# Performance work log

Measured on AMD Instinct MI355X. Metric: run time of the kernel, lower is better.

## Reference

```python
import jax, jax.numpy as jnp
import numpy as np

N_NODES = 100000
N_EDGES = 600000
NODE_DIM = 128
EDGE_DIM = 16
OUT_DIM = 128


def setup_inputs() -> dict:
    key = jax.random.key(0)
    k1, k2, k3, k4 = jax.random.split(key, 4)
    x = jax.random.normal(k1, (N_NODES, NODE_DIM), dtype=jnp.float32)
    edge_index = jax.random.randint(k2, (2, N_EDGES), 0, N_NODES, dtype=jnp.int64)
    edge_attr = jax.random.normal(k3, (N_EDGES, EDGE_DIM), dtype=jnp.float32)
    in_dim = 2 * NODE_DIM + EDGE_DIM
    # Linear layer params (Kaiming-uniform-like scale)
    lim = 1.0 / np.sqrt(in_dim)
    W = jax.random.uniform(k4, (in_dim, OUT_DIM), minval=-lim, maxval=lim, dtype=jnp.float32)
    b = jnp.zeros((OUT_DIM,), dtype=jnp.float32)
    return {"x": x, "edge_index": edge_index, "edge_attr": edge_attr, "W": W, "b": b}


def reference(x, edge_index, edge_attr, W, b):
    # h_ij = Linear([h_i, h_j, x_ij])
    h_i = x[edge_index[0]]            # [E, node_dim]
    h_j = x[edge_index[1]]            # [E, node_dim]
    # Split the GEMM over the concat blocks to avoid materializing [E, 2D+F]
    W_i, W_j, W_e = W[:NODE_DIM], W[NODE_DIM:2 * NODE_DIM], W[2 * NODE_DIM:]
    out = h_i @ W_i + h_j @ W_j + edge_attr @ W_e + b
    return out  # [E, out_dim]
```

## Files before the change

kernel.cpp:

```cpp
#include <hip/hip_runtime.h>
#include <cstdint>
#include <cstddef>

#define NE 600000
#define NN 100000

typedef __attribute__((ext_vector_type(8)))  __bf16         bf16x8;
typedef __attribute__((ext_vector_type(16))) float          f32x16;
typedef __attribute__((ext_vector_type(8)))  unsigned short u16x8;
typedef __attribute__((ext_vector_type(2)))  float          f32x2;

__device__ inline unsigned short f2bf(float f) {
    unsigned int u = __builtin_bit_cast(unsigned int, f);
    u += 0x7fffu + ((u >> 16) & 1u);
    return (unsigned short)(u >> 16);
}

__global__ void pack_w(const float* __restrict__ W, unsigned short* __restrict__ Wp) {
    int t = blockIdx.x * 256 + threadIdx.x;
    if (t >= 272 * 128) return;
    int k = t >> 7, col = t & 127;
    Wp[((k >> 3) * 128 + col) * 8 + (k & 7)] = f2bf(W[t]);
}

__global__ void cvt_x(const float* __restrict__ x, unsigned short* __restrict__ xb) {
    size_t t = (size_t)(blockIdx.x * 256 + threadIdx.x) * 8;
    float4 a = *(const float4*)(x + t);
    float4 b = *(const float4*)(x + t + 4);
    u16x8 o;
    o[0] = f2bf(a.x); o[1] = f2bf(a.y); o[2] = f2bf(a.z); o[3] = f2bf(a.w);
    o[4] = f2bf(b.x); o[5] = f2bf(b.y); o[6] = f2bf(b.z); o[7] = f2bf(b.w);
    *(u16x8*)(xb + t) = o;
}


__global__ __launch_bounds__(256, 2) void node_mm(
    const float* __restrict__ x,
    const unsigned short* __restrict__ Wp,
    float* __restrict__ Y,
    float* __restrict__ Z)
{
    const int lane = threadIdx.x & 63;
    const int wave = threadIdx.x >> 6;
    const int r = lane & 31;
    const int h = lane >> 5;
    const int nb = (blockIdx.x * 4 + wave) * 32;
    if (nb >= NN) return;

    const bf16x8* Wg = (const bf16x8*)Wp;
    f32x16 accY[4], accZ[4];
#pragma unroll
    for (int t = 0; t < 4; ++t)
#pragma unroll
        for (int i = 0; i < 16; ++i) { accY[t][i] = 0.f; accZ[t][i] = 0.f; }

    const float4* ax4 = (const float4*)(x + (size_t)(nb + r) * 128);
#pragma unroll
    for (int S = 0; S < 8; ++S) {
        const int kb = 2 * S + h;
        float4 pp = ax4[kb * 2], qq = ax4[kb * 2 + 1];
        u16x8 o;
        o[0] = f2bf(pp.x); o[1] = f2bf(pp.y); o[2] = f2bf(pp.z); o[3] = f2bf(pp.w);
        o[4] = f2bf(qq.x); o[5] = f2bf(qq.y); o[6] = f2bf(qq.z); o[7] = f2bf(qq.w);
        bf16x8 a = __builtin_bit_cast(bf16x8, o);
#pragma unroll
        for (int t = 0; t < 4; ++t) {
            accY[t] = __builtin_amdgcn_mfma_f32_32x32x16_bf16(
                          a, Wg[kb * 128 + t * 32 + r],        accY[t], 0, 0, 0);
            accZ[t] = __builtin_amdgcn_mfma_f32_32x32x16_bf16(
                          a, Wg[(16 + kb) * 128 + t * 32 + r], accZ[t], 0, 0, 0);
        }
    }

#pragma unroll
    for (int t = 0; t < 4; ++t)
#pragma unroll
        for (int i = 0; i < 16; ++i) {
            int row = (i & 3) + 8 * (i >> 2) + 4 * h;
            Y[(size_t)(nb + row) * 128 + t * 32 + r] = accY[t][i];
            Z[(size_t)(nb + row) * 128 + t * 32 + r] = accZ[t][i];
        }
}

__global__ __launch_bounds__(256, 4) void edge_combine(
    const float* __restrict__ Y,
    const float* __restrict__ Z,
    const int*   __restrict__ ei,
    const float* __restrict__ ea,
    const float* __restrict__ W,
    const float* __restrict__ bias,
    float* __restrict__ out)
{
    const int lane = threadIdx.x & 63;
    const int w = (blockIdx.x * 256 + threadIdx.x) >> 6;
    if (w >= NE / 64) return;
    const int ebase = w * 64;

    f32x2 we[16];
#pragma unroll
    for (int k = 0; k < 16; ++k)
        we[k] = *(const f32x2*)(W + (size_t)(256 + k) * 128 + 2 * lane);
    const f32x2 bv = *(const f32x2*)(bias + 2 * lane);

    const int srcv = ei[ebase + lane];
    const int dstv = ei[NE + ebase + lane];

    int raw[16];
#pragma unroll
    for (int m = 0; m < 16; ++m)
        raw[m] = __builtin_bit_cast(int,
                     ea[(size_t)ebase * 16 + m * 64 + lane]);

    f32x2 yv[8], zv[8];
#pragma unroll
    for (int i = 0; i < 8; ++i) {
        int s = __builtin_amdgcn_readlane(srcv, i);
        int d = __builtin_amdgcn_readlane(dstv, i);
        yv[i] = *(const f32x2*)(Y + ((size_t)s << 7) + 2 * lane);
        zv[i] = *(const f32x2*)(Z + ((size_t)d << 7) + 2 * lane);
    }

#pragma unroll
    for (int j = 0; j < 64; ++j) {
        const int slot = j & 7;
        f32x2 y = yv[slot], z = zv[slot];
        if (j + 8 < 64) {
            int s = __builtin_amdgcn_readlane(srcv, j + 8);
            int d = __builtin_amdgcn_readlane(dstv, j + 8);
            yv[slot] = *(const f32x2*)(Y + ((size_t)s << 7) + 2 * lane);
            zv[slot] = *(const f32x2*)(Z + ((size_t)d << 7) + 2 * lane);
        }
        f32x2 acc = bv;
#pragma unroll
        for (int k = 0; k < 16; ++k) {
            float e = __builtin_bit_cast(float,
                          __builtin_amdgcn_readlane(raw[j >> 2], (j & 3) * 16 + k));
            acc = acc + we[k] * e;
        }
        f32x2 o = acc + y + z;
        __builtin_nontemporal_store(
            o, (f32x2*)(out + ((size_t)(ebase + j) << 7) + 2 * lane));
    }
}


#define WAIT_VM(n) do { asm volatile("" ::: "memory");                      \
                        __builtin_amdgcn_s_waitcnt(0x0F70 | (n));           \
                        asm volatile("" ::: "memory"); } while (0)

__global__ __launch_bounds__(256, 2) void edge_mm2(
    const unsigned short* __restrict__ xb,
    const unsigned short* __restrict__ Wp,
    const int* __restrict__ ei,
    const float* __restrict__ ea,
    const float* __restrict__ bias,
    float* __restrict__ out)
{
    __shared__ __attribute__((aligned(16))) unsigned short Abuf[4][2][32][128];

    const int lane = threadIdx.x & 63;
    const int wave = threadIdx.x >> 6;
    const int r  = lane & 31;
    const int h  = lane >> 5;
    const int g4 = lane >> 4;
    const int sl = lane & 15;
    const int ebase = blockIdx.x * 128 + wave * 32;
    if (ebase >= NE) return;
    const int e = ebase + r;

#pragma unroll
    for (int i = 0; i < 8; ++i) {
        int row = 4 * i + g4;
        int nidx = ei[ebase + row];
        const unsigned short* gs = xb + (size_t)nidx * 128 + ((sl ^ (row & 15)) << 3);
        __builtin_amdgcn_global_load_lds(
            (const __attribute__((address_space(1))) void*)gs,
            (__attribute__((address_space(3))) void*)&Abuf[wave][0][4 * i][0],
            16, 0, 0);
    }
#pragma unroll
    for (int i = 0; i < 8; ++i) {
        int row = 4 * i + g4;
        int nidx = ei[NE + ebase + row];
        const unsigned short* gs = xb + (size_t)nidx * 128 + ((sl ^ (row & 15)) << 3);
        __builtin_amdgcn_global_load_lds(
            (const __attribute__((address_space(1))) void*)gs,
            (__attribute__((address_space(3))) void*)&Abuf[wave][1][4 * i][0],
            16, 0, 0);
    }

    const float4* ae = (const float4*)(ea + (size_t)e * 16);
    float4 p = ae[2 * h], q = ae[2 * h + 1];

    f32x16 acc[4];
#pragma unroll
    for (int t = 0; t < 4; ++t)
#pragma unroll
        for (int i = 0; i < 16; ++i) acc[t][i] = 0.f;

    const bf16x8* Wg = (const bf16x8*)Wp;
    const int rm = r & 15;

    WAIT_VM(8);
#pragma unroll
    for (int S = 0; S < 8; ++S) {
        int kb = 2 * S + h;
        bf16x8 a = *(const bf16x8*)&Abuf[wave][0][r][(kb ^ rm) << 3];
#pragma unroll
        for (int t = 0; t < 4; ++t) {
            bf16x8 b = Wg[kb * 128 + t * 32 + r];
            acc[t] = __builtin_amdgcn_mfma_f32_32x32x16_bf16(a, b, acc[t], 0, 0, 0);
        }
    }

    WAIT_VM(0);
#pragma unroll
    for (int S = 0; S < 8; ++S) {
        int kb = 2 * S + h;
        bf16x8 a = *(const bf16x8*)&Abuf[wave][1][r][(kb ^ rm) << 3];
#pragma unroll
        for (int t = 0; t < 4; ++t) {
            bf16x8 b = Wg[(16 + kb) * 128 + t * 32 + r];
            acc[t] = __builtin_amdgcn_mfma_f32_32x32x16_bf16(a, b, acc[t], 0, 0, 0);
        }
    }

    {
        u16x8 o;
        o[0] = f2bf(p.x); o[1] = f2bf(p.y); o[2] = f2bf(p.z); o[3] = f2bf(p.w);
        o[4] = f2bf(q.x); o[5] = f2bf(q.y); o[6] = f2bf(q.z); o[7] = f2bf(q.w);
        bf16x8 a = __builtin_bit_cast(bf16x8, o);
#pragma unroll
        for (int t = 0; t < 4; ++t) {
            bf16x8 b = Wg[(32 + h) * 128 + t * 32 + r];
            acc[t] = __builtin_amdgcn_mfma_f32_32x32x16_bf16(a, b, acc[t], 0, 0, 0);
        }
    }

    float* orow = out + (size_t)ebase * 128;
#pragma unroll
    for (int t = 0; t < 4; ++t) {
        float bv = bias[t * 32 + r];
#pragma unroll
        for (int i = 0; i < 16; ++i) {
            int row = (i & 3) + 8 * (i >> 2) + 4 * h;
            orow[(size_t)row * 128 + t * 32 + r] = acc[t][i] + bv;
        }
    }
}

__global__ __launch_bounds__(256, 2) void edge_mm_fb(
    const float* __restrict__ x,
    const unsigned short* __restrict__ Wp,
    const int* __restrict__ ei,
    const float* __restrict__ ea,
    const float* __restrict__ bias,
    float* __restrict__ out)
{
    __shared__ unsigned short Wl[32 * 128 * 8];
    {
        const uint4* Wg = (const uint4*)Wp;
        uint4* Ws = (uint4*)Wl;
#pragma unroll
        for (int i = 0; i < 16; ++i)
            Ws[threadIdx.x + 256 * i] = Wg[threadIdx.x + 256 * i];
    }
    const int lane = threadIdx.x & 63;
    const int wave = threadIdx.x >> 6;
    const int r = lane & 31;
    const int h = lane >> 5;
    const long ebase = (long)blockIdx.x * 128 + wave * 32;
    __syncthreads();
    if (ebase >= NE) return;
    const int e = (int)ebase + r;
    const int src = ei[e];
    const int dst = ei[NE + e];
    f32x16 acc[4];
#pragma unroll
    for (int t = 0; t < 4; ++t)
#pragma unroll
        for (int i = 0; i < 16; ++i) acc[t][i] = 0.f;
    const bf16x8* Wv = (const bf16x8*)Wl;
#pragma unroll
    for (int ph = 0; ph < 2; ++ph) {
        int node = ph ? dst : src;
#pragma unroll
        for (int s = 0; s < 8; ++s) {
            const float4* ax = (const float4*)(x + (size_t)node * 128);
            float4 pp = ax[(2 * s + h) * 2], qq = ax[(2 * s + h) * 2 + 1];
            u16x8 o;
            o[0] = f2bf(pp.x); o[1] = f2bf(pp.y); o[2] = f2bf(pp.z); o[3] = f2bf(pp.w);
            o[4] = f2bf(qq.x); o[5] = f2bf(qq.y); o[6] = f2bf(qq.z); o[7] = f2bf(qq.w);
            bf16x8 a = __builtin_bit_cast(bf16x8, o);
            int S = ph * 8 + s;
#pragma unroll
            for (int t = 0; t < 4; ++t) {
                bf16x8 b = Wv[(2 * S + h) * 128 + t * 32 + r];
                acc[t] = __builtin_amdgcn_mfma_f32_32x32x16_bf16(a, b, acc[t], 0, 0, 0);
            }
        }
    }
    {
        const float4* ae = (const float4*)(ea + (size_t)e * 16);
        float4 pp = ae[2 * h], qq = ae[2 * h + 1];
        u16x8 o;
        o[0] = f2bf(pp.x); o[1] = f2bf(pp.y); o[2] = f2bf(pp.z); o[3] = f2bf(pp.w);
        o[4] = f2bf(qq.x); o[5] = f2bf(qq.y); o[6] = f2bf(qq.z); o[7] = f2bf(qq.w);
        bf16x8 a = __builtin_bit_cast(bf16x8, o);
        const bf16x8* Wg = (const bf16x8*)Wp;
#pragma unroll
        for (int t = 0; t < 4; ++t) {
            bf16x8 b = Wg[(32 + h) * 128 + t * 32 + r];
            acc[t] = __builtin_amdgcn_mfma_f32_32x32x16_bf16(a, b, acc[t], 0, 0, 0);
        }
    }
    float* orow = out + (size_t)ebase * 128;
#pragma unroll
    for (int t = 0; t < 4; ++t) {
        float bv = bias[t * 32 + r];
#pragma unroll
        for (int i = 0; i < 16; ++i) {
            int row = (i & 3) + 8 * (i >> 2) + 4 * h;
            orow[(size_t)row * 128 + t * 32 + r] = acc[t][i] + bv;
        }
    }
}

extern "C" void kernel_launch(void* const* d_in, const int* in_sizes, int n_in,
                              void* d_out, int out_size, void* d_ws, size_t ws_size,
                              hipStream_t stream) {
    const float* x  = (const float*)d_in[0];
    const int*   ei = (const int*)d_in[1];
    const float* ea = (const float*)d_in[2];
    const float* W  = (const float*)d_in[3];
    const float* b  = (const float*)d_in[4];
    float* out = (float*)d_out;

    unsigned short* Wp = (unsigned short*)d_ws;
    float* Yb = (float*)((char*)d_ws + 69632);
    float* Zb = (float*)((char*)d_ws + 69632 + 51200000);
    unsigned short* xb = (unsigned short*)((char*)d_ws + 69632);

    const size_t need_mid  = 69632 + (size_t)NN * 128 * 2;
    const size_t need_full = 69632 + 2ull * NN * 128 * 4;

    hipLaunchKernelGGL(pack_w, dim3(136), dim3(256), 0, stream, W, Wp);

    if (ws_size >= need_full) {
        hipLaunchKernelGGL(node_mm, dim3(782), dim3(256), 0, stream, x, Wp, Yb, Zb);
        hipLaunchKernelGGL(edge_combine, dim3(2344), dim3(256), 0, stream,
                           Yb, Zb, ei, ea, W, b, out);
    } else if (ws_size >= need_mid) {
        hipLaunchKernelGGL(cvt_x, dim3(6250), dim3(256), 0, stream, x, xb);
        hipLaunchKernelGGL(edge_mm2, dim3(4688), dim3(256), 0, stream,
                           xb, Wp, ei, ea, b, out);
    } else {
        hipLaunchKernelGGL(edge_mm_fb, dim3(4688), dim3(256), 0, stream,
                           x, Wp, ei, ea, b, out);
    }
}
```

Measured before the change: 503.7 us.

## Rewrite edge combine with async LDS gathers and MFMA edge-attr projection

Replaces the readlane-driven per-edge gather loop with a kernel that handles 16 edges per wave. It gathers the precomputed Y and Z node rows straight into LDS using global_load_lds with an XOR swizzle. The 16-wide edge-attribute projection moves from scalar FMAs with readlane broadcasts to a bf16 16x16x32 MFMA using the packed weights, which lowers precision of that term. The aim is to cut VALU and readlane overhead and raise memory-level parallelism. In exchange it adds LDS use, lowers per-block occupancy bounds, and writes the output as scalar per-element stores.

Result: slower. 536.4 us (+6.5%).

```diff
diff --git a/kernel.cpp b/kernel.cpp
--- a/kernel.cpp
+++ b/kernel.cpp
@@ -7,8 +7,8 @@
 
 typedef __attribute__((ext_vector_type(8)))  __bf16         bf16x8;
 typedef __attribute__((ext_vector_type(16))) float          f32x16;
+typedef __attribute__((ext_vector_type(4)))  float          f32x4;
 typedef __attribute__((ext_vector_type(8)))  unsigned short u16x8;
-typedef __attribute__((ext_vector_type(2)))  float          f32x2;
 
 __device__ inline unsigned short f2bf(float f) {
     unsigned int u = __builtin_bit_cast(unsigned int, f);
@@ -32,6 +32,10 @@
     o[4] = f2bf(b.x); o[5] = f2bf(b.y); o[6] = f2bf(b.z); o[7] = f2bf(b.w);
     *(u16x8*)(xb + t) = o;
 }
+
+#define WAIT_VM(n) do { asm volatile("" ::: "memory");                      \
+                        __builtin_amdgcn_s_waitcnt(0x0F70 | (n));           \
+                        asm volatile("" ::: "memory"); } while (0)
 
 
 __global__ __launch_bounds__(256, 2) void node_mm(
@@ -82,71 +86,95 @@
         }
 }
 
-__global__ __launch_bounds__(256, 4) void edge_combine(
+__global__ __launch_bounds__(256, 2) void edge_combine_lds(
     const float* __restrict__ Y,
     const float* __restrict__ Z,
     const int*   __restrict__ ei,
     const float* __restrict__ ea,
-    const float* __restrict__ W,
+    const unsigned short* __restrict__ Wp,
     const float* __restrict__ bias,
     float* __restrict__ out)
 {
+    __shared__ __attribute__((aligned(16))) float Ybuf[4][16][128];
+    __shared__ __attribute__((aligned(16))) float Zbuf[4][16][128];
+
     const int lane = threadIdx.x & 63;
-    const int w = (blockIdx.x * 256 + threadIdx.x) >> 6;
-    if (w >= NE / 64) return;
-    const int ebase = w * 64;
-
-    f32x2 we[16];
-#pragma unroll
-    for (int k = 0; k < 16; ++k)
-        we[k] = *(const f32x2*)(W + (size_t)(256 + k) * 128 + 2 * lane);
-    const f32x2 bv = *(const f32x2*)(bias + 2 * lane);
-
-    const int srcv = ei[ebase + lane];
-    const int dstv = ei[NE + ebase + lane];
-
-    int raw[16];
-#pragma unroll
-    for (int m = 0; m < 16; ++m)
-        raw[m] = __builtin_bit_cast(int,
-                     ea[(size_t)ebase * 16 + m * 64 + lane]);
-
-    f32x2 yv[8], zv[8];
+    const int wave = threadIdx.x >> 6;
+    const int r16  = lane & 15;
+    const int h4   = lane >> 4;
+    const int e0   = (blockIdx.x * 4 + wave) * 16;
+
+    const float* ear = ea + (size_t)(e0 + r16) * 16 + 8 * (h4 & 1);
+    float4 eaA = *(const float4*)ear;
+    float4 eaB = *(const float4*)(ear + 4);
+    float bvt[8];
+#pragma unroll
+    for (int t = 0; t < 8; ++t) bvt[t] = bias[t * 16 + r16];
+
+    int nidxY[8], nidxZ[8];
+#pragma unroll
+    for (int i = 0; i < 8; ++i) nidxY[i] = ei[e0 + 2 * i + (lane >> 5)];
+#pragma unroll
+    for (int i = 0; i < 8; ++i) nidxZ[i] = ei[NE + e0 + 2 * i + (lane >> 5)];
+
 #pragma unroll
     for (int i = 0; i < 8; ++i) {
-        int s = __builtin_amdgcn_readlane(srcv, i);
-        int d = __builtin_amdgcn_readlane(dstv, i);
-        yv[i] = *(const f32x2*)(Y + ((size_t)s << 7) + 2 * lane);
-        zv[i] = *(const f32x2*)(Z + ((size_t)d << 7) + 2 * lane);
-    }
-
-#pragma unroll
-    for (int j = 0; j < 64; ++j) {
-        const int slot = j & 7;
-        f32x2 y = yv[slot], z = zv[slot];
-        if (j + 8 < 64) {
-            int s = __builtin_amdgcn_readlane(srcv, j + 8);
-            int d = __builtin_amdgcn_readlane(dstv, j + 8);
-            yv[slot] = *(const f32x2*)(Y + ((size_t)s << 7) + 2 * lane);
-            zv[slot] = *(const f32x2*)(Z + ((size_t)d << 7) + 2 * lane);
-        }
-        f32x2 acc = bv;
-#pragma unroll
-        for (int k = 0; k < 16; ++k) {
-            float e = __builtin_bit_cast(float,
-                          __builtin_amdgcn_readlane(raw[j >> 2], (j & 3) * 16 + k));
-            acc = acc + we[k] * e;
-        }
-        f32x2 o = acc + y + z;
-        __builtin_nontemporal_store(
-            o, (f32x2*)(out + ((size_t)(ebase + j) << 7) + 2 * lane));
-    }
-}
-
-
-#define WAIT_VM(n) do { asm volatile("" ::: "memory");                      \
-                        __builtin_amdgcn_s_waitcnt(0x0F70 | (n));           \
-                        asm volatile("" ::: "memory"); } while (0)
+        int row = 2 * i + (lane >> 5);
+        int q = (row >> 2) & 3;
+        const float* gs = Y + ((size_t)nidxY[i] << 7) + (((lane & 31) ^ q) << 2);
+        __builtin_amdgcn_global_load_lds(
+            (const __attribute__((address_space(1))) void*)gs,
+            (__attribute__((address_space(3))) void*)&Ybuf[wave][2 * i][0],
+            16, 0, 0);
+    }
+#pragma unroll
+    for (int i = 0; i < 8; ++i) {
+        int row = 2 * i + (lane >> 5);
+        int q = (row >> 2) & 3;
+        const float* gs = Z + ((size_t)nidxZ[i] << 7) + (((lane & 31) ^ q) << 2);
+        __builtin_amdgcn_global_load_lds(
+            (const __attribute__((address_space(1))) void*)gs,
+            (__attribute__((address_space(3))) void*)&Zbuf[wave][2 * i][0],
+            16, 0, 0);
+    }
+
+    bf16x8 a;
+    {
+        u16x8 o;
+        o[0] = f2bf(eaA.x); o[1] = f2bf(eaA.y); o[2] = f2bf(eaA.z); o[3] = f2bf(eaA.w);
+        o[4] = f2bf(eaB.x); o[5] = f2bf(eaB.y); o[6] = f2bf(eaB.z); o[7] = f2bf(eaB.w);
+        if (h4 >= 2) {
+#pragma unroll
+            for (int j = 0; j < 8; ++j) o[j] = 0;
+        }
+        a = __builtin_bit_cast(bf16x8, o);
+    }
+    const bf16x8* Wg = (const bf16x8*)Wp;
+    f32x4 acc[8];
+#pragma unroll
+    for (int t = 0; t < 8; ++t) {
+        acc[t][0] = bvt[t]; acc[t][1] = bvt[t]; acc[t][2] = bvt[t]; acc[t][3] = bvt[t];
+        bf16x8 b = Wg[(32 + (h4 & 1)) * 128 + t * 16 + r16];
+        acc[t] = __builtin_amdgcn_mfma_f32_16x16x32_bf16(a, b, acc[t], 0, 0, 0);
+    }
+
+    WAIT_VM(0);
+#pragma unroll
+    for (int t = 0; t < 8; ++t) {
+        const int ct = t * 16 + r16;
+        const int fo = ((((ct >> 2) ^ h4) << 2) | (ct & 3));
+#pragma unroll
+        for (int g = 0; g < 4; ++g) {
+            const int er = h4 * 4 + g;
+            float yv = Ybuf[wave][er][fo];
+            float zv = Zbuf[wave][er][fo];
+            __builtin_nontemporal_store(
+                acc[t][g] + yv + zv,
+                out + (size_t)(e0 + er) * 128 + ct);
+        }
+    }
+}
+
 
 __global__ __launch_bounds__(256, 2) void edge_mm2(
     const unsigned short* __restrict__ xb,
@@ -348,8 +376,8 @@
 
     if (ws_size >= need_full) {
         hipLaunchKernelGGL(node_mm, dim3(782), dim3(256), 0, stream, x, Wp, Yb, Zb);
-        hipLaunchKernelGGL(edge_combine, dim3(2344), dim3(256), 0, stream,
-                           Yb, Zb, ei, ea, W, b, out);
+        hipLaunchKernelGGL(edge_combine_lds, dim3(9375), dim3(256), 0, stream,
+                           Yb, Zb, ei, ea, Wp, b, out);
     } else if (ws_size >= need_mid) {
         hipLaunchKernelGGL(cvt_x, dim3(6250), dim3(256), 0, stream, x, xb);
         hipLaunchKernelGGL(edge_mm2, dim3(4688), dim3(256), 0, stream,
```
